# Kernel optimization log

Hardware: AMD Instinct MI355X
Metric: run time of the kernel (lower is better)

Reference implementation:

```python
import jax, jax.numpy as jnp
import numpy as np

B, N, H = 32, 2048, 512
MASK_NEG = 1e30  # matches torch mask_logic constant


def setup_inputs() -> dict:
    key = jax.random.key(0)
    ks = jax.random.split(key, 10)
    Q = jax.random.normal(ks[0], (B, H), dtype=jnp.float32)
    K = jax.random.normal(ks[1], (B, N, H), dtype=jnp.float32)
    V = jax.random.normal(ks[2], (B, N, H), dtype=jnp.float32)
    adj = jax.random.randint(ks[3], (B, N), 0, 2, dtype=jnp.int32)
    s_mask = jax.random.randint(ks[4], (B, N), 0, 2, dtype=jnp.int32)
    s = 1.0 / np.sqrt(H)
    w_att = jax.random.uniform(ks[5], (1, 2 * H), jnp.float32, -s, s)  # nn.Linear(2H,1) weight
    b_att = jax.random.uniform(ks[6], (1,), jnp.float32, -s, s)
    Wr0 = jax.random.uniform(ks[7], (H, H), jnp.float32, -s, s)
    Wr1 = jax.random.uniform(ks[8], (H, H), jnp.float32, -s, s)
    Wri = jax.random.uniform(ks[9], (H, H), jnp.float32, -s, s)
    return {"Q": Q, "K": K, "V": V, "adj": adj, "s_mask": s_mask,
            "w_att": w_att, "b_att": b_att, "Wr0": Wr0, "Wr1": Wr1, "Wri": Wri}


def reference(Q, K, V, adj, s_mask, w_att, b_att, Wr0, Wr1, Wri):
    Hdim = Q.shape[-1]
    # additive score: linear(cat(Q_exp, K)) split into Q-part + K-part (avoids materializing [B,N,2H])
    wq, wk = w_att[:, :Hdim], w_att[:, Hdim:]          # [1,H] each
    alpha = (Q @ wq[0]) [:, None] + K @ wk[0] + b_att[0]  # [B,N]
    # adjacency mask + softmax over neighbors
    masked = alpha - (1.0 - adj.astype(jnp.float32)) * MASK_NEG
    attn = jax.nn.softmax(masked, axis=1)               # [B,N]
    # gated value projection: V0 where s_mask==1, V1 where 0
    V0 = jnp.einsum('bnh,oh->bno', V, Wr0)
    V1 = jnp.einsum('bnh,oh->bno', V, Wr1)
    sm = s_mask.astype(jnp.float32)[..., None]          # [B,N,1]
    Vm = V0 * sm + V1 * (1.0 - sm)
    # weighted aggregation + residual projection
    attn_sum = jnp.einsum('bn,bnh->bh', attn, Vm) + Q @ Wri.T
    return attn[:, None, :], attn_sum                   # ([B,1,N], [B,H])
```

## Files before the change

kernel.cpp:

```cpp
#include <hip/hip_runtime.h>

#define BB 32
#define NN 2048
#define HH 512

static __device__ __forceinline__ float dot4(float4 a, float4 b) {
    return a.x * b.x + a.y * b.y + a.z * b.z + a.w * b.w;
}


__global__ void k_scores(const float* __restrict__ K,
                         const float* __restrict__ w_att,
                         const int* __restrict__ adj,
                         float* __restrict__ scores) {
    int wave = (blockIdx.x * blockDim.x + threadIdx.x) >> 6;
    int lane = threadIdx.x & 63;
    const float* wk = w_att + HH;
    float4 a0 = *(const float4*)(wk + lane * 4);
    float4 a1 = *(const float4*)(wk + 256 + lane * 4);
    int row0 = wave * 4;
    const float* Kb = K + (size_t)row0 * HH + lane * 4;
    float4 k00 = *(const float4*)(Kb);
    float4 k01 = *(const float4*)(Kb + 256);
    float4 k10 = *(const float4*)(Kb + HH);
    float4 k11 = *(const float4*)(Kb + HH + 256);
    float4 k20 = *(const float4*)(Kb + 2 * HH);
    float4 k21 = *(const float4*)(Kb + 2 * HH + 256);
    float4 k30 = *(const float4*)(Kb + 3 * HH);
    float4 k31 = *(const float4*)(Kb + 3 * HH + 256);
    float s0 = dot4(k00, a0) + dot4(k01, a1);
    float s1 = dot4(k10, a0) + dot4(k11, a1);
    float s2 = dot4(k20, a0) + dot4(k21, a1);
    float s3 = dot4(k30, a0) + dot4(k31, a1);
#pragma unroll
    for (int off = 32; off > 0; off >>= 1) {
        s0 += __shfl_down(s0, off, 64);
        s1 += __shfl_down(s1, off, 64);
        s2 += __shfl_down(s2, off, 64);
        s3 += __shfl_down(s3, off, 64);
    }
    if (lane == 0) {
        int4 a = *(const int4*)(adj + row0);
        float4 o;
        o.x = a.x ? s0 : -1e30f;
        o.y = a.y ? s1 : -1e30f;
        o.z = a.z ? s2 : -1e30f;
        o.w = a.w ? s3 : -1e30f;
        *(float4*)(scores + row0) = o;
    }
}

#define CH 16
__global__ void k_wsum(const float* __restrict__ V,
                       const float* __restrict__ scores,
                       float* __restrict__ attn,
                       const int* __restrict__ s_mask,
                       float* __restrict__ u0,
                       float* __restrict__ u1) {
    int b = blockIdx.x >> 5;
    int hc = (blockIdx.x & 31) * CH;
    int t = threadIdx.x;
    __shared__ float red[4];
    __shared__ float2 wls[NN];
    __shared__ float part[4][4][8];

    const float* srow = scores + b * NN;
    float4 va = *(const float4*)(srow + t * 8);
    float4 vb = *(const float4*)(srow + t * 8 + 4);
    float m = fmaxf(fmaxf(fmaxf(va.x, va.y), fmaxf(va.z, va.w)),
                    fmaxf(fmaxf(vb.x, vb.y), fmaxf(vb.z, vb.w)));
#pragma unroll
    for (int off = 32; off > 0; off >>= 1) m = fmaxf(m, __shfl_xor(m, off, 64));
    if ((t & 63) == 0) red[t >> 6] = m;
    __syncthreads();
    float m4 = fmaxf(fmaxf(red[0], red[1]), fmaxf(red[2], red[3]));
    float e0 = expf(va.x - m4), e1 = expf(va.y - m4);
    float e2 = expf(va.z - m4), e3 = expf(va.w - m4);
    float e4 = expf(vb.x - m4), e5 = expf(vb.y - m4);
    float e6 = expf(vb.z - m4), e7 = expf(vb.w - m4);
    float sum = ((e0 + e1) + (e2 + e3)) + ((e4 + e5) + (e6 + e7));
#pragma unroll
    for (int off = 32; off > 0; off >>= 1) sum += __shfl_xor(sum, off, 64);
    __syncthreads();
    if ((t & 63) == 0) red[t >> 6] = sum;
    __syncthreads();
    float inv = 1.0f / (red[0] + red[1] + red[2] + red[3]);

    float w0 = e0 * inv, w1 = e1 * inv, w2 = e2 * inv, w3 = e3 * inv;
    float w4 = e4 * inv, w5 = e5 * inv, w6 = e6 * inv, w7 = e7 * inv;
    if (hc == 0) {
        float4 oa = {w0, w1, w2, w3};
        float4 ob = {w4, w5, w6, w7};
        *(float4*)(attn + b * NN + t * 8) = oa;
        *(float4*)(attn + b * NN + t * 8 + 4) = ob;
    }
    int4 sa = *(const int4*)(s_mask + b * NN + t * 8);
    int4 sb = *(const int4*)(s_mask + b * NN + t * 8 + 4);
    int i8 = t * 8;
    wls[i8 + 0] = sa.x ? make_float2(w0, 0.f) : make_float2(0.f, w0);
    wls[i8 + 1] = sa.y ? make_float2(w1, 0.f) : make_float2(0.f, w1);
    wls[i8 + 2] = sa.z ? make_float2(w2, 0.f) : make_float2(0.f, w2);
    wls[i8 + 3] = sa.w ? make_float2(w3, 0.f) : make_float2(0.f, w3);
    wls[i8 + 4] = sb.x ? make_float2(w4, 0.f) : make_float2(0.f, w4);
    wls[i8 + 5] = sb.y ? make_float2(w5, 0.f) : make_float2(0.f, w5);
    wls[i8 + 6] = sb.z ? make_float2(w6, 0.f) : make_float2(0.f, w6);
    wls[i8 + 7] = sb.w ? make_float2(w7, 0.f) : make_float2(0.f, w7);
    __syncthreads();

    int col = t & 3;
    int rowg = t >> 2;
    const float* Vb = V + (size_t)b * NN * HH + hc + col * 4;
    float4 A0 = {0, 0, 0, 0}, A1 = {0, 0, 0, 0};
#pragma unroll 8
    for (int i = 0; i < 32; i++) {
        int n = rowg + (i << 6);
        float4 x = *(const float4*)(Vb + (size_t)n * HH);
        float2 w = wls[n];
        A0.x += w.x * x.x; A0.y += w.x * x.y; A0.z += w.x * x.z; A0.w += w.x * x.w;
        A1.x += w.y * x.x; A1.y += w.y * x.y; A1.z += w.y * x.z; A1.w += w.y * x.w;
    }
#pragma unroll
    for (int off = 32; off >= 4; off >>= 1) {
        A0.x += __shfl_down(A0.x, off, 64); A0.y += __shfl_down(A0.y, off, 64);
        A0.z += __shfl_down(A0.z, off, 64); A0.w += __shfl_down(A0.w, off, 64);
        A1.x += __shfl_down(A1.x, off, 64); A1.y += __shfl_down(A1.y, off, 64);
        A1.z += __shfl_down(A1.z, off, 64); A1.w += __shfl_down(A1.w, off, 64);
    }
    int wv = t >> 6;
    if ((t & 63) < 4) {
        float* p = part[wv][t & 3];
        p[0] = A0.x; p[1] = A0.y; p[2] = A0.z; p[3] = A0.w;
        p[4] = A1.x; p[5] = A1.y; p[6] = A1.z; p[7] = A1.w;
    }
    __syncthreads();
    if (t < 4) {
        float4 r0 = {0, 0, 0, 0}, r1 = {0, 0, 0, 0};
#pragma unroll
        for (int w = 0; w < 4; w++) {
            const float* p = part[w][t];
            r0.x += p[0]; r0.y += p[1]; r0.z += p[2]; r0.w += p[3];
            r1.x += p[4]; r1.y += p[5]; r1.z += p[6]; r1.w += p[7];
        }
        *(float4*)(u0 + b * HH + hc + t * 4) = r0;
        *(float4*)(u1 + b * HH + hc + t * 4) = r1;
    }
}

__global__ void k_out(const float* __restrict__ Q,
                      const float* __restrict__ Wr0,
                      const float* __restrict__ Wr1,
                      const float* __restrict__ Wri,
                      const float* __restrict__ u0,
                      const float* __restrict__ u1,
                      float* __restrict__ out) {
    int wave = (blockIdx.x * blockDim.x + threadIdx.x) >> 6;
    int lane = threadIdx.x & 63;
    if (wave >= BB * HH) return;
    int b = wave >> 9;
    int o = wave & 511;
    const float* q = Q + b * HH;
    const float* x0 = u0 + b * HH;
    const float* x1 = u1 + b * HH;
    const float* r0 = Wr0 + (size_t)o * HH;
    const float* r1 = Wr1 + (size_t)o * HH;
    const float* ri = Wri + (size_t)o * HH;
    float s = 0.0f;
#pragma unroll
    for (int part = 0; part < 2; part++) {
        int h = part * 256 + lane * 4;
        s += dot4(*(const float4*)(r0 + h), *(const float4*)(x0 + h));
        s += dot4(*(const float4*)(r1 + h), *(const float4*)(x1 + h));
        s += dot4(*(const float4*)(ri + h), *(const float4*)(q + h));
    }
#pragma unroll
    for (int off = 32; off > 0; off >>= 1) s += __shfl_down(s, off, 64);
    if (lane == 0) out[wave] = s;
}

extern "C" void kernel_launch(void* const* d_in, const int* in_sizes, int n_in,
                              void* d_out, int out_size, void* d_ws, size_t ws_size,
                              hipStream_t stream) {
    const float* Q = (const float*)d_in[0];
    const float* K = (const float*)d_in[1];
    const float* V = (const float*)d_in[2];
    const int* adj = (const int*)d_in[3];
    const int* s_mask = (const int*)d_in[4];
    const float* w_att = (const float*)d_in[5];
    const float* Wr0 = (const float*)d_in[7];
    const float* Wr1 = (const float*)d_in[8];
    const float* Wri = (const float*)d_in[9];

    float* out = (float*)d_out;
    float* attn = out;
    float* attn_sum = out + BB * NN;
    float* ws = (float*)d_ws;
    float* u0 = ws;
    float* u1 = ws + BB * HH;
    float* scores = ws + 2 * BB * HH;

    k_scores<<<(BB * NN) / 16, 256, 0, stream>>>(K, w_att, adj, scores);
    k_wsum<<<BB * (HH / CH), 256, 0, stream>>>(V, scores, attn, s_mask, u0, u1);
    k_out<<<(BB * HH) / 4, 256, 0, stream>>>(Q, Wr0, Wr1, Wri, u0, u1, attn_sum);
}
```

Baseline: 313.7 us.

## Split weighted V sum over row chunks with atomic accumulation instead of column slices

The V aggregation kernel now gives each block 64 rows of the sequence across all 512 hidden columns, rather than 16 columns across all 2048 rows. Each thread reads a contiguous float4 along the row, so accesses coalesce into full rows. Partial sums are merged across blocks with float atomicAdd into u0 and u1, which the scores kernel now zeroes. The cost is many atomics, nondeterministic summation order, and every block still recomputing the full softmax max and sum over 2048 scores.

After: 303.6 us. 1.03x faster.

```diff
diff --git a/kernel.cpp b/kernel.cpp
--- a/kernel.cpp
+++ b/kernel.cpp
@@ -12,8 +12,11 @@
 __global__ void k_scores(const float* __restrict__ K,
                          const float* __restrict__ w_att,
                          const int* __restrict__ adj,
-                         float* __restrict__ scores) {
-    int wave = (blockIdx.x * blockDim.x + threadIdx.x) >> 6;
+                         float* __restrict__ scores,
+                         float* __restrict__ ws) {
+    int gtid = blockIdx.x * blockDim.x + threadIdx.x;
+    if (gtid < 2 * BB * HH) ws[gtid] = 0.0f;
+    int wave = gtid >> 6;
     int lane = threadIdx.x & 63;
     const float* wk = w_att + HH;
     float4 a0 = *(const float4*)(wk + lane * 4);
@@ -50,7 +53,7 @@
     }
 }
 
-#define CH 16
+#define ROWS 64
 __global__ void k_wsum(const float* __restrict__ V,
                        const float* __restrict__ scores,
                        float* __restrict__ attn,
@@ -58,11 +61,11 @@
                        float* __restrict__ u0,
                        float* __restrict__ u1) {
     int b = blockIdx.x >> 5;
-    int hc = (blockIdx.x & 31) * CH;
+    int n0 = (blockIdx.x & 31) * ROWS;
     int t = threadIdx.x;
     __shared__ float red[4];
-    __shared__ float2 wls[NN];
-    __shared__ float part[4][4][8];
+    __shared__ float2 wls[ROWS];
+    __shared__ float comb[1024];
 
     const float* srow = scores + b * NN;
     float4 va = *(const float4*)(srow + t * 8);
@@ -74,11 +77,9 @@
     if ((t & 63) == 0) red[t >> 6] = m;
     __syncthreads();
     float m4 = fmaxf(fmaxf(red[0], red[1]), fmaxf(red[2], red[3]));
-    float e0 = expf(va.x - m4), e1 = expf(va.y - m4);
-    float e2 = expf(va.z - m4), e3 = expf(va.w - m4);
-    float e4 = expf(vb.x - m4), e5 = expf(vb.y - m4);
-    float e6 = expf(vb.z - m4), e7 = expf(vb.w - m4);
-    float sum = ((e0 + e1) + (e2 + e3)) + ((e4 + e5) + (e6 + e7));
+    float sum = expf(va.x - m4) + expf(va.y - m4) + expf(va.z - m4) +
+                expf(va.w - m4) + expf(vb.x - m4) + expf(vb.y - m4) +
+                expf(vb.z - m4) + expf(vb.w - m4);
 #pragma unroll
     for (int off = 32; off > 0; off >>= 1) sum += __shfl_xor(sum, off, 64);
     __syncthreads();
@@ -86,63 +87,41 @@
     __syncthreads();
     float inv = 1.0f / (red[0] + red[1] + red[2] + red[3]);
 
-    float w0 = e0 * inv, w1 = e1 * inv, w2 = e2 * inv, w3 = e3 * inv;
-    float w4 = e4 * inv, w5 = e5 * inv, w6 = e6 * inv, w7 = e7 * inv;
-    if (hc == 0) {
-        float4 oa = {w0, w1, w2, w3};
-        float4 ob = {w4, w5, w6, w7};
-        *(float4*)(attn + b * NN + t * 8) = oa;
-        *(float4*)(attn + b * NN + t * 8 + 4) = ob;
+    if (t < ROWS) {
+        float w = expf(srow[n0 + t] - m4) * inv;
+        attn[b * NN + n0 + t] = w;
+        int sm = s_mask[b * NN + n0 + t];
+        wls[t] = sm ? make_float2(w, 0.0f) : make_float2(0.0f, w);
     }
-    int4 sa = *(const int4*)(s_mask + b * NN + t * 8);
-    int4 sb = *(const int4*)(s_mask + b * NN + t * 8 + 4);
-    int i8 = t * 8;
-    wls[i8 + 0] = sa.x ? make_float2(w0, 0.f) : make_float2(0.f, w0);
-    wls[i8 + 1] = sa.y ? make_float2(w1, 0.f) : make_float2(0.f, w1);
-    wls[i8 + 2] = sa.z ? make_float2(w2, 0.f) : make_float2(0.f, w2);
-    wls[i8 + 3] = sa.w ? make_float2(w3, 0.f) : make_float2(0.f, w3);
-    wls[i8 + 4] = sb.x ? make_float2(w4, 0.f) : make_float2(0.f, w4);
-    wls[i8 + 5] = sb.y ? make_float2(w5, 0.f) : make_float2(0.f, w5);
-    wls[i8 + 6] = sb.z ? make_float2(w6, 0.f) : make_float2(0.f, w6);
-    wls[i8 + 7] = sb.w ? make_float2(w7, 0.f) : make_float2(0.f, w7);
     __syncthreads();
 
-    int col = t & 3;
-    int rowg = t >> 2;
-    const float* Vb = V + (size_t)b * NN * HH + hc + col * 4;
+    int h4 = (t & 127) * 4;
+    int half = t >> 7;
+    const float* Vb = V + (size_t)(b * NN + n0 + half * 32) * HH + h4;
     float4 A0 = {0, 0, 0, 0}, A1 = {0, 0, 0, 0};
 #pragma unroll 8
     for (int i = 0; i < 32; i++) {
-        int n = rowg + (i << 6);
-        float4 x = *(const float4*)(Vb + (size_t)n * HH);
-        float2 w = wls[n];
+        float4 x = *(const float4*)(Vb + (size_t)i * HH);
+        float2 w = wls[half * 32 + i];
         A0.x += w.x * x.x; A0.y += w.x * x.y; A0.z += w.x * x.z; A0.w += w.x * x.w;
         A1.x += w.y * x.x; A1.y += w.y * x.y; A1.z += w.y * x.z; A1.w += w.y * x.w;
     }
-#pragma unroll
-    for (int off = 32; off >= 4; off >>= 1) {
-        A0.x += __shfl_down(A0.x, off, 64); A0.y += __shfl_down(A0.y, off, 64);
-        A0.z += __shfl_down(A0.z, off, 64); A0.w += __shfl_down(A0.w, off, 64);
-        A1.x += __shfl_down(A1.x, off, 64); A1.y += __shfl_down(A1.y, off, 64);
-        A1.z += __shfl_down(A1.z, off, 64); A1.w += __shfl_down(A1.w, off, 64);
-    }
-    int wv = t >> 6;
-    if ((t & 63) < 4) {
-        float* p = part[wv][t & 3];
-        p[0] = A0.x; p[1] = A0.y; p[2] = A0.z; p[3] = A0.w;
-        p[4] = A1.x; p[5] = A1.y; p[6] = A1.z; p[7] = A1.w;
+    if (half == 1) {
+        int i8 = (t - 128) * 8;
+        comb[i8 + 0] = A0.x; comb[i8 + 1] = A0.y; comb[i8 + 2] = A0.z; comb[i8 + 3] = A0.w;
+        comb[i8 + 4] = A1.x; comb[i8 + 5] = A1.y; comb[i8 + 6] = A1.z; comb[i8 + 7] = A1.w;
     }
     __syncthreads();
-    if (t < 4) {
-        float4 r0 = {0, 0, 0, 0}, r1 = {0, 0, 0, 0};
-#pragma unroll
-        for (int w = 0; w < 4; w++) {
-            const float* p = part[w][t];
-            r0.x += p[0]; r0.y += p[1]; r0.z += p[2]; r0.w += p[3];
-            r1.x += p[4]; r1.y += p[5]; r1.z += p[6]; r1.w += p[7];
-        }
-        *(float4*)(u0 + b * HH + hc + t * 4) = r0;
-        *(float4*)(u1 + b * HH + hc + t * 4) = r1;
+    if (half == 0) {
+        int i8 = t * 8;
+        A0.x += comb[i8 + 0]; A0.y += comb[i8 + 1]; A0.z += comb[i8 + 2]; A0.w += comb[i8 + 3];
+        A1.x += comb[i8 + 4]; A1.y += comb[i8 + 5]; A1.z += comb[i8 + 6]; A1.w += comb[i8 + 7];
+        float* p0 = u0 + b * HH + h4;
+        float* p1 = u1 + b * HH + h4;
+        atomicAdd(p0 + 0, A0.x); atomicAdd(p0 + 1, A0.y);
+        atomicAdd(p0 + 2, A0.z); atomicAdd(p0 + 3, A0.w);
+        atomicAdd(p1 + 0, A1.x); atomicAdd(p1 + 1, A1.y);
+        atomicAdd(p1 + 2, A1.z); atomicAdd(p1 + 3, A1.w);
     }
 }
 
@@ -198,7 +177,7 @@
     float* u1 = ws + BB * HH;
     float* scores = ws + 2 * BB * HH;
 
-    k_scores<<<(BB * NN) / 16, 256, 0, stream>>>(K, w_att, adj, scores);
-    k_wsum<<<BB * (HH / CH), 256, 0, stream>>>(V, scores, attn, s_mask, u0, u1);
+    k_scores<<<(BB * NN) / 16, 256, 0, stream>>>(K, w_att, adj, scores, ws);
+    k_wsum<<<BB * 32, 256, 0, stream>>>(V, scores, attn, s_mask, u0, u1);
     k_out<<<(BB * HH) / 4, 256, 0, stream>>>(Q, Wr0, Wr1, Wri, u0, u1, attn_sum);
 }
```
